# Kernel tuning notes

Hardware: AMD Instinct MI355X
Metric: run time of the kernel (lower is better)

Reference implementation:

```python
import jax, jax.numpy as jnp
import numpy as np

EPS = 1e-5

def _bn_train(h, gamma, beta):
    # training-mode BatchNorm2d: stats over (N, H, W), biased variance
    m = h.mean(axis=(0, 2, 3), keepdims=True)
    v = ((h - m) ** 2).mean(axis=(0, 2, 3), keepdims=True)
    return gamma[None, :, None, None] * (h - m) / jnp.sqrt(v + EPS) + beta[None, :, None, None]

def _box_conv(h, x_min, x_max, y_min, y_max):
    # h: (B, Cbt, H, W); box params: (Cbt, nb). Output: (B, Cbt*nb, H, W).
    # Continuous box-sum via 2D integral image + bilinear interpolation of the
    # (piecewise-bilinear) cumulative integral at fractional box corners,
    # with zero padding outside the image (== clamping integral-image coords).
    B, Cc, H, W = h.shape
    nb = x_min.shape[1]
    K = Cc * nb
    II = jnp.pad(jnp.cumsum(jnp.cumsum(h, axis=2), axis=3),
                 ((0, 0), (0, 0), (1, 0), (1, 0)))  # (B, Cc, H+1, W+1)
    cidx = jnp.arange(K) // nb                      # input channel per out channel
    IIc = II[:, cidx]                               # (B, K, H+1, W+1)
    rows = jnp.arange(H, dtype=h.dtype)
    cols = jnp.arange(W, dtype=h.dtype)
    u_lo = x_min.reshape(-1)
    u_hi = x_max.reshape(-1) + 1.0
    v_lo = y_min.reshape(-1)
    v_hi = y_max.reshape(-1) + 1.0

    def F(u_off, v_off):
        # bilinear sample of IIc at continuous coords (i + u_off[k], j + v_off[k])
        u = jnp.clip(rows[None, :] + u_off[:, None], 0.0, float(H))  # (K, H)
        v = jnp.clip(cols[None, :] + v_off[:, None], 0.0, float(W))  # (K, W)
        u0f = jnp.floor(u); au = u - u0f
        v0f = jnp.floor(v); av = v - v0f
        u0 = u0f.astype(jnp.int32); u1 = jnp.minimum(u0 + 1, H)
        v0 = v0f.astype(jnp.int32); v1 = jnp.minimum(v0 + 1, W)
        R0 = jnp.take_along_axis(IIc, u0[None, :, :, None], axis=2)  # (B,K,H,W+1)
        R1 = jnp.take_along_axis(IIc, u1[None, :, :, None], axis=2)
        R = R0 * (1.0 - au)[None, :, :, None] + R1 * au[None, :, :, None]
        C0 = jnp.take_along_axis(R, v0[None, :, None, :], axis=3)    # (B,K,H,W)
        C1 = jnp.take_along_axis(R, v1[None, :, None, :], axis=3)
        return C0 * (1.0 - av)[None, :, None, :] + C1 * av[None, :, None, :]

    return F(u_hi, v_hi) - F(u_lo, v_hi) - F(u_hi, v_lo) + F(u_lo, v_lo)

def setup_inputs() -> dict:
    key = jax.random.key(0)
    ks = jax.random.split(key, 8)
    B, C, H, W = 4, 128, 160, 160
    nb = 4
    Cbt = C // nb
    x = jax.random.normal(ks[0], (B, C, H, W), dtype=jnp.float32)
    w1 = jax.random.normal(ks[1], (Cbt, C), dtype=jnp.float32) * (1.0 / np.sqrt(C))
    g1 = jnp.ones((Cbt,), jnp.float32)
    b1 = jnp.zeros((Cbt,), jnp.float32)
    # random learnable boxes within [-H/2, H/2]
    x_min = -jax.random.uniform(ks[2], (Cbt, nb), jnp.float32, 1.0, H / 2.0)
    x_max = jax.random.uniform(ks[3], (Cbt, nb), jnp.float32, 1.0, H / 2.0)
    y_min = -jax.random.uniform(ks[4], (Cbt, nb), jnp.float32, 1.0, W / 2.0)
    y_max = jax.random.uniform(ks[5], (Cbt, nb), jnp.float32, 1.0, W / 2.0)
    g2 = jnp.ones((C,), jnp.float32)
    b2 = jnp.zeros((C,), jnp.float32)
    return {"x": x, "w1": w1, "g1": g1, "b1": b1,
            "x_min": x_min, "x_max": x_max, "y_min": y_min, "y_max": y_max,
            "g2": g2, "b2": b2}

def reference(x, w1, g1, b1, x_min, x_max, y_min, y_max, g2, b2):
    # 1x1 conv (no bias) -> BN -> ReLU
    h = jnp.einsum('oc,bchw->bohw', w1, x)
    h = jax.nn.relu(_bn_train(h, g1, b1))
    # learned box convolution (integral-image box sums, normalize=False default)
    h = _box_conv(h, x_min, x_max, y_min, y_max)
    # BN -> (Dropout p=0 is identity) -> residual ReLU
    h = _bn_train(h, g2, b2)
    return jax.nn.relu(x + h)
```

## Files before the change

### kernel.cpp

```cpp
#include <hip/hip_runtime.h>
#include <cstdint>

constexpr int B  = 4;
constexpr int C  = 128;
constexpr int CM = 32;
constexpr int H  = 160;
constexpr int W  = 160;
constexpr int HW = H * W;
constexpr int HP = H + 1;
constexpr int WP = W + 1;
constexpr int PLANE = HP * WP;
constexpr int TY = 16;
constexpr int NTILE = H / TY;
constexpr int PB  = 64;
constexpr int K1B = B * HW / PB;
constexpr int NB2 = B * NTILE;
constexpr int QR = 40;

__global__ __launch_bounds__(256) void k_transpose_w(
    const float* __restrict__ w1, float* __restrict__ wTg)
{
    int t = blockIdx.x * 256 + threadIdx.x;
    if (t < C * CM) {
        int o = t / C, c = t % C;
        wTg[c * CM + o] = w1[t];
    }
}

__global__ __launch_bounds__(256) void k_conv(
    const float* __restrict__ x, const float* __restrict__ wTg,
    float* __restrict__ h, float* __restrict__ part1)
{
    __shared__ float part[4 * CM * PB];
    int tid = threadIdx.x;
    int wave = tid >> 6, lane = tid & 63;
    int bid = blockIdx.x;
    int b = bid / 400;
    int p0 = (bid % 400) * PB;

    int wq = __builtin_amdgcn_readfirstlane(wave);
    const float* xb = x + (size_t)b * C * HW + (size_t)(wq * 32) * HW + p0 + lane;
    const float* wrow = wTg + (size_t)(wq * 32) * CM;

    float acc[CM];
    #pragma unroll
    for (int o = 0; o < CM; ++o) acc[o] = 0.f;

    #pragma unroll 4
    for (int i = 0; i < 32; ++i) {
        float xv = xb[(size_t)i * HW];
        const float* wr = wrow + i * CM;
        #pragma unroll
        for (int o = 0; o < CM; ++o)
            acc[o] = fmaf(wr[o], xv, acc[o]);
    }

    float* pq = &part[wave * CM * PB];
    #pragma unroll
    for (int o = 0; o < CM; ++o) pq[o * PB + lane] = acc[o];
    __syncthreads();

    int o  = tid >> 3;
    int l0 = (tid & 7) * 8;
    const float* pp = &part[o * PB + l0];
    float4 f0 = *reinterpret_cast<const float4*>(pp);
    float4 f1 = *reinterpret_cast<const float4*>(pp + 4);
    #pragma unroll
    for (int q = 1; q < 4; ++q) {
        const float4 a0 = *reinterpret_cast<const float4*>(pp + q * CM * PB);
        const float4 a1 = *reinterpret_cast<const float4*>(pp + q * CM * PB + 4);
        f0.x += a0.x; f0.y += a0.y; f0.z += a0.z; f0.w += a0.w;
        f1.x += a1.x; f1.y += a1.y; f1.z += a1.z; f1.w += a1.w;
    }

    float* hb = h + ((size_t)(b * CM + o)) * HW + p0 + l0;
    *reinterpret_cast<float4*>(hb)     = f0;
    *reinterpret_cast<float4*>(hb + 4) = f1;

    float s  = f0.x + f0.y + f0.z + f0.w + f1.x + f1.y + f1.z + f1.w;
    float s2 = f0.x * f0.x + f0.y * f0.y + f0.z * f0.z + f0.w * f0.w
             + f1.x * f1.x + f1.y * f1.y + f1.z * f1.z + f1.w * f1.w;
    #pragma unroll
    for (int off = 4; off > 0; off >>= 1) {
        s  += __shfl_down(s,  off, 8);
        s2 += __shfl_down(s2, off, 8);
    }
    if ((tid & 7) == 0) {
        part1[(size_t)o * K1B + bid]        = s;
        part1[(size_t)(o + CM) * K1B + bid] = s2;
    }
}

__global__ __launch_bounds__(256) void k_rowsum1(
    const float* __restrict__ part1, double* __restrict__ rowsum1)
{
    __shared__ double red[256];
    int tid = threadIdx.x;
    int r = blockIdx.x;
    const float* row = part1 + (size_t)r * K1B;
    double a = 0.0;
    for (int i = tid; i < K1B; i += 256) a += (double)row[i];
    red[tid] = a;
    __syncthreads();
    #pragma unroll
    for (int s = 128; s > 0; s >>= 1) {
        if (tid < s) red[tid] += red[tid + s];
        __syncthreads();
    }
    if (tid == 0) rowsum1[r] = red[0];
}

__global__ __launch_bounds__(256) void k_scan_part(
    const float* __restrict__ h, const double* __restrict__ rowsum1,
    const float* __restrict__ g1, const float* __restrict__ b1,
    float* __restrict__ II, float* __restrict__ qlast)
{
    __shared__ float buf[QR * W];
    int tid = threadIdx.x;
    int wave = tid >> 6, lane = tid & 63;
    int blk = blockIdx.x;
    int plane = blk >> 2, q = blk & 3;
    int cm = plane & (CM - 1);

    double n = (double)(B * HW);
    double mean = rowsum1[cm] / n;
    double var  = rowsum1[CM + cm] / n - mean * mean;
    float inv   = (float)(1.0 / sqrt(var + 1e-5));
    float scale = g1[cm] * inv;
    float shift = b1[cm] - (float)mean * scale;

    const float* hp = h + (size_t)plane * HW + (size_t)q * QR * W;
    float* IIp = II + (size_t)plane * PLANE;

    if (q == 0) {
        for (int e = tid; e < WP; e += 256) IIp[e] = 0.f;
    }

    for (int y = wave; y < QR; y += 4) {
        const float* hr = hp + (size_t)y * W;
        float carry = 0.f;
        #pragma unroll
        for (int x0 = 0; x0 < W; x0 += 64) {
            int xx = x0 + lane;
            float v = (xx < W) ? fmaxf(fmaf(scale, hr[xx], shift), 0.f) : 0.f;
            #pragma unroll
            for (int off = 1; off < 64; off <<= 1) {
                float t = __shfl_up(v, off);
                if (lane >= off) v += t;
            }
            v += carry;
            if (xx < W) buf[y * W + xx] = v;
            carry = __shfl(v, 63);
        }
    }
    __syncthreads();

    float* op = IIp + (size_t)(q * QR + 1) * WP;
    float* ql = qlast + ((size_t)plane * 3 + q) * WP;
    if (tid <= W) {
        float run = 0.f;
        #pragma unroll 4
        for (int r = 0; r < QR; ++r) {
            float v = 0.f;
            if (tid > 0) { run += buf[r * W + (tid - 1)]; v = run; }
            op[(size_t)r * WP + tid] = v;
            if (r == QR - 1 && q < 3) ql[tid] = v;
        }
    }
}

__global__ __launch_bounds__(256) void k_scan_fix(
    float* __restrict__ II, const float* __restrict__ qlast)
{
    __shared__ float off[WP];
    int tid = threadIdx.x;
    int blk = blockIdx.x;
    int plane = blk / 3, f = blk % 3;

    const float* qb = qlast + (size_t)plane * 3 * WP;
    for (int v = tid; v < WP; v += 256) {
        float s = qb[v];
        if (f >= 1) s += qb[WP + v];
        if (f >= 2) s += qb[2 * WP + v];
        off[v] = s;
    }
    __syncthreads();

    float* P = II + (size_t)plane * PLANE + (size_t)(41 + f * QR) * WP;
    constexpr int total = QR * WP;
    for (int e = tid; e < total; e += 256) {
        P[e] += off[e % WP];
    }
}

struct BoxSmem {
    float D[TY][WP];
    int   ru0[2][TY];
    int   ru1[2][TY];
    float rua[2][TY];
    int   cv0[2][W];
    float cva[2][W];
};

__device__ inline void fill_D(BoxSmem& sm, const float* __restrict__ II,
    int tile, int k, int b,
    const float* __restrict__ xmin, const float* __restrict__ xmax,
    const float* __restrict__ ymin, const float* __restrict__ ymax)
{
    int tid = threadIdx.x;
    if (tid < 2 * TY) {
        int side = tid / TY, ty = tid % TY;
        float off = side ? (xmax[k] + 1.f) : xmin[k];
        float u = fminf(fmaxf((float)(tile * TY + ty) + off, 0.f), 160.f);
        float uf = floorf(u);
        int i0 = (int)uf;
        sm.ru0[side][ty] = i0;
        sm.ru1[side][ty] = min(i0 + 1, 160);
        sm.rua[side][ty] = u - uf;
    }
    for (int e = tid; e < 2 * W; e += 256) {
        int side = e / W, xx = e % W;
        float off = side ? (ymax[k] + 1.f) : ymin[k];
        float v = fminf(fmaxf((float)xx + off, 0.f), 160.f);
        float vf = floorf(v);
        sm.cv0[side][xx] = (int)vf;
        sm.cva[side][xx] = v - vf;
    }
    __syncthreads();

    const float* P = II + (size_t)(b * CM + (k >> 2)) * PLANE;
    for (int e = tid; e < TY * WP; e += 256) {
        int ty = e / WP, v = e % WP;
        float al = sm.rua[0][ty], ah = sm.rua[1][ty];
        float lo = P[(size_t)sm.ru0[0][ty] * WP + v] * (1.f - al)
                 + P[(size_t)sm.ru1[0][ty] * WP + v] * al;
        float hi = P[(size_t)sm.ru0[1][ty] * WP + v] * (1.f - ah)
                 + P[(size_t)sm.ru1[1][ty] * WP + v] * ah;
        sm.D[ty][v] = hi - lo;
    }
    __syncthreads();
}

__device__ inline float eval_D(const BoxSmem& sm, int ty, int xx)
{
    int   l0 = sm.cv0[0][xx];
    float la = sm.cva[0][xx];
    int   l1 = min(l0 + 1, 160);
    int   h0 = sm.cv0[1][xx];
    float ha = sm.cva[1][xx];
    int   h1 = min(h0 + 1, 160);
    const float* Dr = sm.D[ty];
    return (Dr[h0] * (1.f - ha) + Dr[h1] * ha)
         - (Dr[l0] * (1.f - la) + Dr[l1] * la);
}

__global__ __launch_bounds__(256) void k_box_part(
    const float* __restrict__ II,
    const float* __restrict__ xmin, const float* __restrict__ xmax,
    const float* __restrict__ ymin, const float* __restrict__ ymax,
    float* __restrict__ part2)
{
    __shared__ BoxSmem sm;
    __shared__ float red[4][2];
    int tile = blockIdx.x, k = blockIdx.y, b = blockIdx.z;
    fill_D(sm, II, tile, k, b, xmin, xmax, ymin, ymax);

    float s = 0.f, s2 = 0.f;
    for (int o = threadIdx.x; o < TY * W; o += 256) {
        int ty = o / W, xx = o % W;
        float v = eval_D(sm, ty, xx);
        s  += v;
        s2 += v * v;
    }
    #pragma unroll
    for (int off = 32; off > 0; off >>= 1) {
        s  += __shfl_down(s,  off);
        s2 += __shfl_down(s2, off);
    }
    int wave = threadIdx.x >> 6, lane = threadIdx.x & 63;
    if (lane == 0) { red[wave][0] = s; red[wave][1] = s2; }
    __syncthreads();
    if (threadIdx.x == 0) {
        int idx = b * NTILE + tile;
        part2[(size_t)k * NB2 + idx]       = red[0][0] + red[1][0] + red[2][0] + red[3][0];
        part2[(size_t)(C + k) * NB2 + idx] = red[0][1] + red[1][1] + red[2][1] + red[3][1];
    }
}

__global__ __launch_bounds__(256) void k_reduce2(
    const float* __restrict__ part2, const float* __restrict__ g2,
    const float* __restrict__ b2, float* __restrict__ sc2)
{
    __shared__ double dsum[2 * C];
    int t = threadIdx.x;
    const float4* rp = reinterpret_cast<const float4*>(part2 + (size_t)t * NB2);
    double acc = 0.0;
    #pragma unroll
    for (int i = 0; i < NB2 / 4; ++i) {
        float4 v = rp[i];
        acc += (double)v.x + (double)v.y + (double)v.z + (double)v.w;
    }
    dsum[t] = acc;
    __syncthreads();
    if (t < C) {
        double n = (double)(B * HW);
        double mean = dsum[t] / n;
        double var  = dsum[C + t] / n - mean * mean;
        float inv   = (float)(1.0 / sqrt(var + 1e-5));
        float scale = g2[t] * inv;
        sc2[t]     = scale;
        sc2[C + t] = b2[t] - (float)mean * scale;
    }
}

__global__ __launch_bounds__(256) void k_box_final(
    const float* __restrict__ II, const float* __restrict__ x,
    const float* __restrict__ xmin, const float* __restrict__ xmax,
    const float* __restrict__ ymin, const float* __restrict__ ymax,
    const float* __restrict__ sc2, float* __restrict__ out)
{
    __shared__ BoxSmem sm;
    int tile = blockIdx.x, k = blockIdx.y, b = blockIdx.z;
    fill_D(sm, II, tile, k, b, xmin, xmax, ymin, ymax);

    float scale = sc2[k], shift = sc2[C + k];
    size_t base = ((size_t)(b * C + k)) * HW + (size_t)tile * TY * W;
    for (int o = threadIdx.x; o < TY * W; o += 256) {
        int ty = o / W, xx = o % W;
        float v = eval_D(sm, ty, xx);
        size_t idx = base + (size_t)ty * W + xx;
        out[idx] = fmaxf(x[idx] + fmaf(scale, v, shift), 0.f);
    }
}

extern "C" void kernel_launch(void* const* d_in, const int* in_sizes, int n_in,
                              void* d_out, int out_size, void* d_ws, size_t ws_size,
                              hipStream_t stream)
{
    const float* x    = (const float*)d_in[0];
    const float* w1   = (const float*)d_in[1];
    const float* g1   = (const float*)d_in[2];
    const float* b1   = (const float*)d_in[3];
    const float* xmin = (const float*)d_in[4];
    const float* xmax = (const float*)d_in[5];
    const float* ymin = (const float*)d_in[6];
    const float* ymax = (const float*)d_in[7];
    const float* g2   = (const float*)d_in[8];
    const float* b2   = (const float*)d_in[9];
    float* out = (float*)d_out;

    char* ws = (char*)d_ws;
    float* sc2 = (float*)ws;
    float* wTg = (float*)(ws + 1280);
    double* rowsum1 = (double*)(ws + 17664);
    float* h   = (float*)(ws + 20480);
    float* II  = (float*)(ws + 20480 + (size_t)B * CM * HW * sizeof(float));
    float* qlast = (float*)(ws + 20480 + (size_t)B * CM * HW * sizeof(float)
                               + (size_t)B * CM * PLANE * sizeof(float));
    float* part1 = II;
    float* part2 = h;

    k_transpose_w<<<dim3((C * CM + 255) / 256), 256, 0, stream>>>(w1, wTg);
    k_conv     <<<dim3(K1B), 256, 0, stream>>>(x, wTg, h, part1);
    k_rowsum1  <<<dim3(2 * CM), 256, 0, stream>>>(part1, rowsum1);
    k_scan_part<<<dim3(B * CM * 4), 256, 0, stream>>>(h, rowsum1, g1, b1, II, qlast);
    k_scan_fix <<<dim3(B * CM * 3), 256, 0, stream>>>(II, qlast);
    k_box_part <<<dim3(NTILE, C, B), 256, 0, stream>>>(II, xmin, xmax, ymin, ymax, part2);
    k_reduce2  <<<dim3(1), 256, 0, stream>>>(part2, g2, b2, sc2);
    k_box_final<<<dim3(NTILE, C, B), 256, 0, stream>>>(II, x, xmin, xmax, ymin, ymax,
                                                       sc2, out);
}
```

Measured before the change: 111.8 us.

## Fold scan-fix carry offsets into box kernels and drop k_scan_fix launch

Result: faster. 103.1 us (-7.7%).

```diff
diff --git a/kernel.cpp b/kernel.cpp
--- a/kernel.cpp
+++ b/kernel.cpp
@@ -169,54 +169,50 @@
     }
 }
 
-__global__ __launch_bounds__(256) void k_scan_fix(
-    float* __restrict__ II, const float* __restrict__ qlast)
-{
-    __shared__ float off[WP];
-    int tid = threadIdx.x;
-    int blk = blockIdx.x;
-    int plane = blk / 3, f = blk % 3;
-
-    const float* qb = qlast + (size_t)plane * 3 * WP;
-    for (int v = tid; v < WP; v += 256) {
-        float s = qb[v];
-        if (f >= 1) s += qb[WP + v];
-        if (f >= 2) s += qb[2 * WP + v];
-        off[v] = s;
-    }
-    __syncthreads();
-
-    float* P = II + (size_t)plane * PLANE + (size_t)(41 + f * QR) * WP;
-    constexpr int total = QR * WP;
-    for (int e = tid; e < total; e += 256) {
-        P[e] += off[e % WP];
-    }
-}
-
 struct BoxSmem {
     float D[TY][WP];
+    float coff[4][WP];
     int   ru0[2][TY];
     int   ru1[2][TY];
     float rua[2][TY];
+    int   rq0[2][TY];
+    int   rq1[2][TY];
     int   cv0[2][W];
     float cva[2][W];
 };
 
+__device__ inline int qidx(int row) { return row == 0 ? 0 : (row - 1) / QR; }
+
 __device__ inline void fill_D(BoxSmem& sm, const float* __restrict__ II,
+    const float* __restrict__ qlast,
     int tile, int k, int b,
     const float* __restrict__ xmin, const float* __restrict__ xmax,
     const float* __restrict__ ymin, const float* __restrict__ ymax)
 {
     int tid = threadIdx.x;
+    int plane = b * CM + (k >> 2);
     if (tid < 2 * TY) {
         int side = tid / TY, ty = tid % TY;
         float off = side ? (xmax[k] + 1.f) : xmin[k];
         float u = fminf(fmaxf((float)(tile * TY + ty) + off, 0.f), 160.f);
         float uf = floorf(u);
         int i0 = (int)uf;
+        int i1 = min(i0 + 1, 160);
         sm.ru0[side][ty] = i0;
-        sm.ru1[side][ty] = min(i0 + 1, 160);
+        sm.ru1[side][ty] = i1;
         sm.rua[side][ty] = u - uf;
+        sm.rq0[side][ty] = qidx(i0);
+        sm.rq1[side][ty] = qidx(i1);
+    }
+    {
+        const float* qb = qlast + (size_t)plane * 3 * WP;
+        for (int v = tid; v < WP; v += 256) {
+            float l0 = qb[v], l1 = qb[WP + v], l2 = qb[2 * WP + v];
+            sm.coff[0][v] = 0.f;
+            sm.coff[1][v] = l0;
+            sm.coff[2][v] = l0 + l1;
+            sm.coff[3][v] = l0 + l1 + l2;
+        }
     }
     for (int e = tid; e < 2 * W; e += 256) {
         int side = e / W, xx = e % W;
@@ -228,15 +224,17 @@
     }
     __syncthreads();
 
-    const float* P = II + (size_t)(b * CM + (k >> 2)) * PLANE;
+    const float* P = II + (size_t)plane * PLANE;
+    int ty = tid / WP, v = tid % WP;
     for (int e = tid; e < TY * WP; e += 256) {
-        int ty = e / WP, v = e % WP;
         float al = sm.rua[0][ty], ah = sm.rua[1][ty];
-        float lo = P[(size_t)sm.ru0[0][ty] * WP + v] * (1.f - al)
-                 + P[(size_t)sm.ru1[0][ty] * WP + v] * al;
-        float hi = P[(size_t)sm.ru0[1][ty] * WP + v] * (1.f - ah)
-                 + P[(size_t)sm.ru1[1][ty] * WP + v] * ah;
+        float lo = (P[(size_t)sm.ru0[0][ty] * WP + v] + sm.coff[sm.rq0[0][ty]][v]) * (1.f - al)
+                 + (P[(size_t)sm.ru1[0][ty] * WP + v] + sm.coff[sm.rq1[0][ty]][v]) * al;
+        float hi = (P[(size_t)sm.ru0[1][ty] * WP + v] + sm.coff[sm.rq0[1][ty]][v]) * (1.f - ah)
+                 + (P[(size_t)sm.ru1[1][ty] * WP + v] + sm.coff[sm.rq1[1][ty]][v]) * ah;
         sm.D[ty][v] = hi - lo;
+        ty += 1; v += 95;
+        if (v >= WP) { v -= WP; ty += 1; }
     }
     __syncthreads();
 }
@@ -255,7 +253,7 @@
 }
 
 __global__ __launch_bounds__(256) void k_box_part(
-    const float* __restrict__ II,
+    const float* __restrict__ II, const float* __restrict__ qlast,
     const float* __restrict__ xmin, const float* __restrict__ xmax,
     const float* __restrict__ ymin, const float* __restrict__ ymax,
     float* __restrict__ part2)
@@ -263,24 +261,28 @@
     __shared__ BoxSmem sm;
     __shared__ float red[4][2];
     int tile = blockIdx.x, k = blockIdx.y, b = blockIdx.z;
-    fill_D(sm, II, tile, k, b, xmin, xmax, ymin, ymax);
-
+    fill_D(sm, II, qlast, tile, k, b, xmin, xmax, ymin, ymax);
+
+    int tid = threadIdx.x;
     float s = 0.f, s2 = 0.f;
-    for (int o = threadIdx.x; o < TY * W; o += 256) {
-        int ty = o / W, xx = o % W;
+    int ty = tid / W, xx = tid % W;
+    #pragma unroll
+    for (int i = 0; i < TY * W / 256; ++i) {
         float v = eval_D(sm, ty, xx);
         s  += v;
         s2 += v * v;
+        ty += 1; xx += 96;
+        if (xx >= W) { xx -= W; ty += 1; }
     }
     #pragma unroll
     for (int off = 32; off > 0; off >>= 1) {
         s  += __shfl_down(s,  off);
         s2 += __shfl_down(s2, off);
     }
-    int wave = threadIdx.x >> 6, lane = threadIdx.x & 63;
+    int wave = tid >> 6, lane = tid & 63;
     if (lane == 0) { red[wave][0] = s; red[wave][1] = s2; }
     __syncthreads();
-    if (threadIdx.x == 0) {
+    if (tid == 0) {
         int idx = b * NTILE + tile;
         part2[(size_t)k * NB2 + idx]       = red[0][0] + red[1][0] + red[2][0] + red[3][0];
         part2[(size_t)(C + k) * NB2 + idx] = red[0][1] + red[1][1] + red[2][1] + red[3][1];
@@ -314,22 +316,27 @@
 }
 
 __global__ __launch_bounds__(256) void k_box_final(
-    const float* __restrict__ II, const float* __restrict__ x,
+    const float* __restrict__ II, const float* __restrict__ qlast,
+    const float* __restrict__ x,
     const float* __restrict__ xmin, const float* __restrict__ xmax,
     const float* __restrict__ ymin, const float* __restrict__ ymax,
     const float* __restrict__ sc2, float* __restrict__ out)
 {
     __shared__ BoxSmem sm;
     int tile = blockIdx.x, k = blockIdx.y, b = blockIdx.z;
-    fill_D(sm, II, tile, k, b, xmin, xmax, ymin, ymax);
-
+    fill_D(sm, II, qlast, tile, k, b, xmin, xmax, ymin, ymax);
+
+    int tid = threadIdx.x;
     float scale = sc2[k], shift = sc2[C + k];
     size_t base = ((size_t)(b * C + k)) * HW + (size_t)tile * TY * W;
-    for (int o = threadIdx.x; o < TY * W; o += 256) {
-        int ty = o / W, xx = o % W;
+    int ty = tid / W, xx = tid % W;
+    #pragma unroll
+    for (int i = 0; i < TY * W / 256; ++i) {
         float v = eval_D(sm, ty, xx);
-        size_t idx = base + (size_t)ty * W + xx;
+        size_t idx = base + tid + 256 * i;
         out[idx] = fmaxf(x[idx] + fmaf(scale, v, shift), 0.f);
+        ty += 1; xx += 96;
+        if (xx >= W) { xx -= W; ty += 1; }
     }
 }
 
@@ -364,9 +371,8 @@
     k_conv     <<<dim3(K1B), 256, 0, stream>>>(x, wTg, h, part1);
     k_rowsum1  <<<dim3(2 * CM), 256, 0, stream>>>(part1, rowsum1);
     k_scan_part<<<dim3(B * CM * 4), 256, 0, stream>>>(h, rowsum1, g1, b1, II, qlast);
-    k_scan_fix <<<dim3(B * CM * 3), 256, 0, stream>>>(II, qlast);
-    k_box_part <<<dim3(NTILE, C, B), 256, 0, stream>>>(II, xmin, xmax, ymin, ymax, part2);
+    k_box_part <<<dim3(NTILE, C, B), 256, 0, stream>>>(II, qlast, xmin, xmax, ymin, ymax, part2);
     k_reduce2  <<<dim3(1), 256, 0, stream>>>(part2, g2, b2, sc2);
-    k_box_final<<<dim3(NTILE, C, B), 256, 0, stream>>>(II, x, xmin, xmax, ymin, ymax,
+    k_box_final<<<dim3(NTILE, C, B), 256, 0, stream>>>(II, qlast, x, xmin, xmax, ymin, ymax,
                                                        sc2, out);
 }
```
